# Optimization experiments

Hardware: AMD Instinct MI355X
Metric: run time of the kernel (lower is better)

The kernel has to match this reference:

```python
import jax, jax.numpy as jnp
import numpy as np

B, IN, HID, OUT = 1024, 512, 128, 64
INP1 = IN + 1  # 513, after prepending ones column


def setup_inputs() -> dict:
    key = jax.random.key(0)
    k1, k2, k3, k4, k5, k6, k7, k8 = jax.random.split(key, 8)
    s1 = 1.0 / np.sqrt(INP1 * INP1)
    s2 = 1.0 / np.sqrt(HID)
    return {
        "img": jax.random.normal(k1, (B, IN), dtype=jnp.float32),
        "tab": jax.random.normal(k2, (B, IN), dtype=jnp.float32),
        "W1": jax.random.uniform(k3, (HID, INP1 * INP1), jnp.float32, -s1, s1),
        "b1": jax.random.uniform(k4, (HID,), jnp.float32, -s1, s1),
        "W2": jax.random.uniform(k5, (HID, HID), jnp.float32, -s2, s2),
        "b2": jax.random.uniform(k6, (HID,), jnp.float32, -s2, s2),
        "W3": jax.random.uniform(k7, (OUT, HID), jnp.float32, -s2, s2),
        "b3": jax.random.uniform(k8, (OUT,), jnp.float32, -s2, s2),
    }


def reference(img, tab, W1, b1, W2, b2, W3, b3):
    ones = jnp.ones((img.shape[0], 1), dtype=img.dtype)
    x = jnp.concatenate([ones, img], axis=1)  # [B, IN+1]
    t = jnp.concatenate([ones, tab], axis=1)  # [B, IN+1]
    # batched outer product, flattened: [B, (IN+1)*(IN+1)]
    fusion = jnp.einsum("bi,bj->bij", x, t).reshape(x.shape[0], -1)
    # dropout is identity in eval mode
    y1 = fusion @ W1.T + b1
    y2 = jnp.tanh(y1 @ W2.T + b2)
    y3 = jax.nn.relu(y2 @ W3.T + b3)
    return y3
```

## Files before the change

kernel.cpp:

```cpp
#include <hip/hip_runtime.h>
#include <hip/hip_bf16.h>

typedef __bf16 bf16x8 __attribute__((ext_vector_type(8)));
typedef float f32x4 __attribute__((ext_vector_type(4)));
typedef float f32x4u __attribute__((ext_vector_type(4), aligned(4)));
typedef unsigned short u16x8 __attribute__((ext_vector_type(8)));

typedef __attribute__((address_space(1))) const unsigned int gu32;
typedef __attribute__((address_space(3))) unsigned int lu32;

#define B_SZ   1024
#define IN_SZ  512
#define HID    128
#define OUT_SZ 64
#define BK     32
#define NKT    16
#define M2     65536

static __device__ __forceinline__ unsigned short f2bf(float f) {
    __hip_bfloat16 h = __float2bfloat16(f);
    return *reinterpret_cast<unsigned short*>(&h);
}

__global__ __launch_bounds__(256) void prep_kernel(
    const float* __restrict__ img, const float* __restrict__ tab,
    unsigned short* __restrict__ tbt, float* __restrict__ xhT,
    float* __restrict__ tc)
{
    const int blk = blockIdx.x;
    for (int j = threadIdx.x; j < 512; j += 256) {
        float v = (j == 0) ? 1.0f : tab[(size_t)blk * IN_SZ + (j - 1)];
        tbt[(size_t)blk * 512 + j] = f2bf(v);
    }
    if (threadIdx.x == 0) tc[blk] = tab[(size_t)blk * IN_SZ + 511];
    if (blk < 513) {
        for (int b = threadIdx.x; b < B_SZ; b += 256)
            xhT[(size_t)blk * B_SZ + b] =
                (blk == 0) ? 1.0f : img[(size_t)b * IN_SZ + (blk - 1)];
    }
}

__global__ __launch_bounds__(256) void prep2_kernel(
    const float* __restrict__ w1, unsigned short* __restrict__ w1c)
{
    const long long gid = (long long)blockIdx.x * 256 + threadIdx.x;
    const int r  = (int)(gid >> 6);
    const int c8 = ((int)gid & 63) << 3;
    const size_t srow = (size_t)(r >> 9) * 513 + (r & 511);
    const float* src = w1 + srow * 513 + c8;
    const f32x4u lo = *reinterpret_cast<const f32x4u*>(src);
    const f32x4u hi = *reinterpret_cast<const f32x4u*>(src + 4);
    u16x8 u;
    u[0] = f2bf(lo[0]); u[1] = f2bf(lo[1]); u[2] = f2bf(lo[2]); u[3] = f2bf(lo[3]);
    u[4] = f2bf(hi[0]); u[5] = f2bf(hi[1]); u[6] = f2bf(hi[2]); u[7] = f2bf(hi[3]);
    *reinterpret_cast<u16x8*>(w1c + (size_t)r * 512 + c8) = u;
}

__global__ __launch_bounds__(256) void prep3_kernel(
    const float* __restrict__ w1, float* __restrict__ wrowT)
{
    const int idx = blockIdx.x * 256 + threadIdx.x;
    if (idx < 513 * 128) {
        const int j = idx >> 7, h = idx & 127;
        wrowT[idx] = w1[((size_t)h * 513 + 512) * 513 + j];
    }
}

__global__ __launch_bounds__(512, 4) void gemm_fused(
    const float* __restrict__ w1, const unsigned short* __restrict__ w1c,
    const unsigned short* __restrict__ tbt,
    const float* __restrict__ xhT, const float* __restrict__ tc,
    float* __restrict__ y1acc)
{
    __shared__ unsigned short Als[3][128 * BK];
    __shared__ unsigned short Bls[3][256 * BK];

    const int wgid = (blockIdx.x & 7) * 256 + (blockIdx.x >> 3);
    const int bm = wgid >> 2;
    const int bn = wgid & 3;
    const int m0 = bm * 128;
    const int n0 = bn * 256;
    const int tid  = threadIdx.x;
    const int wv   = tid >> 6;
    const int wr   = wv >> 2;
    const int wc   = wv & 3;
    const int lane = tid & 63;
    const int l15  = lane & 15;
    const int kg   = lane >> 4;

    const unsigned short* asrc;
    {
        const int r  = tid >> 2;
        const int cl = (tid & 3) ^ ((r >> 1) & 3);
        asrc = w1c + (size_t)(m0 + r) * 512 + cl * 8;
    }
    const int aBase = (wv * 64) * 8;

    const unsigned short* bsrc[2];
    int bBase[2];
    #pragma unroll
    for (int q = 0; q < 2; ++q) {
        const int p  = q * 512 + tid;
        const int r  = p >> 2;
        const int cl = (p & 3) ^ ((r >> 1) & 3);
        bsrc[q] = tbt + (size_t)(n0 + r) * 512 + cl * 8;
        bBase[q] = (q * 512 + wv * 64) * 8;
    }

    int aoffs[4], boffs[4];
    #pragma unroll
    for (int ms = 0; ms < 4; ++ms) {
        const int r = wr * 64 + ms * 16 + l15;
        aoffs[ms] = (r * 4 + (kg ^ ((r >> 1) & 3))) * 8;
    }
    #pragma unroll
    for (int ns = 0; ns < 4; ++ns) {
        const int r = wc * 64 + ns * 16 + l15;
        boffs[ns] = (r * 4 + (kg ^ ((r >> 1) & 3))) * 8;
    }

    f32x4 acc[4][4] = {};

#define STAGE(BUF, KT) do {                                                  \
        const int k32_ = (KT) * BK;                                          \
        __builtin_amdgcn_global_load_lds(                                    \
            (gu32*)(const void*)(asrc + k32_),                               \
            (lu32*)(void*)&Als[BUF][aBase], 16, 0, 0);                       \
        _Pragma("unroll")                                                    \
        for (int q_ = 0; q_ < 2; ++q_)                                       \
            __builtin_amdgcn_global_load_lds(                                \
                (gu32*)(const void*)(bsrc[q_] + k32_),                       \
                (lu32*)(void*)&Bls[BUF][bBase[q_]], 16, 0, 0);               \
    } while (0)

    STAGE(0, 0);
    STAGE(1, 1);

    #pragma unroll
    for (int kt = 0; kt < NKT; ++kt) {
        if (kt == NKT - 1) asm volatile("s_waitcnt vmcnt(0)" ::: "memory");
        else               asm volatile("s_waitcnt vmcnt(3)" ::: "memory");
        __builtin_amdgcn_s_barrier();
        __builtin_amdgcn_sched_barrier(0);

        if (kt + 2 < NKT) STAGE((kt + 2) % 3, kt + 2);

        const int cur = kt % 3;
        const unsigned short* ab = &Als[cur][0];
        const unsigned short* bb = &Bls[cur][0];
        bf16x8 af[4], bfr[4];
        #pragma unroll
        for (int ms = 0; ms < 4; ++ms)
            af[ms] = *reinterpret_cast<const bf16x8*>(&ab[aoffs[ms]]);
        #pragma unroll
        for (int ns = 0; ns < 4; ++ns)
            bfr[ns] = *reinterpret_cast<const bf16x8*>(&bb[boffs[ns]]);
        __builtin_amdgcn_s_setprio(1);
        #pragma unroll
        for (int ms = 0; ms < 4; ++ms)
            #pragma unroll
            for (int ns = 0; ns < 4; ++ns)
                acc[ms][ns] = __builtin_amdgcn_mfma_f32_16x16x32_bf16(
                    af[ms], bfr[ns], acc[ms][ns], 0, 0, 0);
        __builtin_amdgcn_s_setprio(0);
    }
#undef STAGE

    const int h0    = bm >> 2;
    const int ibase = (bm & 3) * 128;
    const size_t orow = (size_t)h0 * 513;

    float wcv[4][4];
    #pragma unroll
    for (int ms = 0; ms < 4; ++ms)
        #pragma unroll
        for (int v = 0; v < 4; ++v) {
            const int i_ = ibase + wr * 64 + ms * 16 + kg * 4 + v;
            wcv[ms][v] = w1[(orow + i_) * 513 + 512];
        }

    #pragma unroll
    for (int ns = 0; ns < 4; ++ns) {
        const int ncol = n0 + wc * 64 + ns * 16 + l15;
        const float tv = tc[ncol];
        float s0 = 0.f;
        #pragma unroll
        for (int ms = 0; ms < 4; ++ms) {
            const int i_ = ibase + wr * 64 + ms * 16 + kg * 4;
            #pragma unroll
            for (int v = 0; v < 4; ++v)
                s0 += (acc[ms][ns][v] + wcv[ms][v] * tv)
                      * xhT[(size_t)(i_ + v) * B_SZ + ncol];
        }
        s0 += __shfl_xor(s0, 16); s0 += __shfl_xor(s0, 32);
        if (lane < 16) atomicAdd(&y1acc[(size_t)ncol * HID + h0], s0);
    }
}

__global__ __launch_bounds__(128) void tail_kernel(
    const float* __restrict__ img, const float* __restrict__ tab,
    const float* __restrict__ wrowT, float* __restrict__ y1acc)
{
    __shared__ float tls[4][513];
    const int b0 = blockIdx.x * 4;
    const int h  = threadIdx.x;
    #pragma unroll
    for (int q = 0; q < 4; ++q)
        for (int j = h; j < 513; j += 128)
            tls[q][j] = (j == 0) ? 1.0f : tab[(size_t)(b0 + q) * IN_SZ + (j - 1)];
    __syncthreads();
    float a0 = 0.f, a1 = 0.f, a2 = 0.f, a3 = 0.f;
    #pragma unroll 8
    for (int j = 0; j < 513; ++j) {
        const float w = wrowT[j * 128 + h];
        a0 += w * tls[0][j]; a1 += w * tls[1][j];
        a2 += w * tls[2][j]; a3 += w * tls[3][j];
    }
    atomicAdd(&y1acc[(size_t)(b0 + 0) * HID + h], a0 * img[(size_t)(b0 + 0) * IN_SZ + 511]);
    atomicAdd(&y1acc[(size_t)(b0 + 1) * HID + h], a1 * img[(size_t)(b0 + 1) * IN_SZ + 511]);
    atomicAdd(&y1acc[(size_t)(b0 + 2) * HID + h], a2 * img[(size_t)(b0 + 2) * IN_SZ + 511]);
    atomicAdd(&y1acc[(size_t)(b0 + 3) * HID + h], a3 * img[(size_t)(b0 + 3) * IN_SZ + 511]);
}

__global__ __launch_bounds__(512, 4) void gemm_fused_fb(
    const float* __restrict__ w1, const unsigned short* __restrict__ tbt,
    const float* __restrict__ xhT, const float* __restrict__ tc,
    float* __restrict__ y1acc)
{
    __shared__ float          Afs[2][64 * BK];
    __shared__ unsigned short Bls[2][512 * BK];

    const int bm = blockIdx.x >> 1;
    const int bn = blockIdx.x & 1;
    const int m0 = bm * 64;
    const int n0 = bn * 512;
    const int tid  = threadIdx.x;
    const int wv   = tid >> 6;
    const int lane = tid & 63;
    const int l15  = lane & 15;
    const int kg   = lane >> 4;

    const int ar  = tid >> 3;
    const int acl = (tid & 7) ^ (ar & 7);
    const float* asrc = w1 + (size_t)(m0 + ar) * 513 + acl * 4;
    const int aBase = (wv * 64) * 4;

    const unsigned short* bsrc[4];
    int bBase[4];
    #pragma unroll
    for (int q = 0; q < 4; ++q) {
        const int p  = q * 512 + tid;
        const int r  = p >> 2;
        const int cl = (p & 3) ^ ((r >> 1) & 3);
        bsrc[q] = tbt + (size_t)(n0 + r) * 512 + cl * 8;
        bBase[q] = (q * 512 + wv * 64) * 8;
    }

    int aoff0[4], aoff1[4], boffs[4];
    #pragma unroll
    for (int ms = 0; ms < 4; ++ms) {
        const int r = ms * 16 + l15;
        aoff0[ms] = r * 32 + (((kg * 2) + 0) ^ (r & 7)) * 4;
        aoff1[ms] = r * 32 + (((kg * 2) + 1) ^ (r & 7)) * 4;
    }
    #pragma unroll
    for (int ns = 0; ns < 4; ++ns) {
        const int r = wv * 64 + ns * 16 + l15;
        boffs[ns] = ((r << 2) | (kg ^ ((r >> 1) & 3))) * 8;
    }

    f32x4 acc[4][4] = {};

#define STAGE_FB(BUF, KT) do {                                               \
        const int k32_ = (KT) * BK;                                          \
        _Pragma("unroll")                                                    \
        for (int q_ = 0; q_ < 4; ++q_)                                       \
            __builtin_amdgcn_global_load_lds(                                \
                (gu32*)(const void*)(bsrc[q_] + k32_),                       \
                (lu32*)(void*)&Bls[BUF][bBase[q_]], 16, 0, 0);               \
        __builtin_amdgcn_global_load_lds(                                    \
            (gu32*)(const void*)(asrc + k32_),                               \
            (lu32*)(void*)&Afs[BUF][aBase], 16, 0, 0);                       \
    } while (0)

    STAGE_FB(0, 0);
    __syncthreads();

    for (int kt = 0; kt < NKT; ++kt) {
        const int cur = kt & 1;
        if (kt + 1 < NKT) STAGE_FB(cur ^ 1, kt + 1);

        const float*          ab = &Afs[cur][0];
        const unsigned short* bb = &Bls[cur][0];
        bf16x8 bfr[4];
        #pragma unroll
        for (int ns = 0; ns < 4; ++ns)
            bfr[ns] = *reinterpret_cast<const bf16x8*>(&bb[boffs[ns]]);
        #pragma unroll
        for (int ms = 0; ms < 4; ++ms) {
            const f32x4 lo = *reinterpret_cast<const f32x4*>(&ab[aoff0[ms]]);
            const f32x4 hi = *reinterpret_cast<const f32x4*>(&ab[aoff1[ms]]);
            u16x8 u;
            u[0] = f2bf(lo[0]); u[1] = f2bf(lo[1]);
            u[2] = f2bf(lo[2]); u[3] = f2bf(lo[3]);
            u[4] = f2bf(hi[0]); u[5] = f2bf(hi[1]);
            u[6] = f2bf(hi[2]); u[7] = f2bf(hi[3]);
            const bf16x8 af = __builtin_bit_cast(bf16x8, u);
            #pragma unroll
            for (int ns = 0; ns < 4; ++ns)
                acc[ms][ns] = __builtin_amdgcn_mfma_f32_16x16x32_bf16(
                    af, bfr[ns], acc[ms][ns], 0, 0, 0);
        }
        __syncthreads();
    }
#undef STAGE_FB

    const int h0 = m0 / 513;
    const int mb = (h0 + 1) * 513;
    const bool cross = (mb < m0 + 64);

    float wcv[4][4];
    #pragma unroll
    for (int ms = 0; ms < 4; ++ms)
        #pragma unroll
        for (int v = 0; v < 4; ++v)
            wcv[ms][v] = w1[(size_t)(m0 + ms * 16 + kg * 4 + v) * 513 + 512];

    #pragma unroll
    for (int ns = 0; ns < 4; ++ns) {
        const int ncol = n0 + wv * 64 + ns * 16 + l15;
        const float tv = tc[ncol];
        float s0 = 0.f, s1 = 0.f;
        #pragma unroll
        for (int ms = 0; ms < 4; ++ms) {
            #pragma unroll
            for (int v = 0; v < 4; ++v) {
                const int m = m0 + ms * 16 + kg * 4 + v;
                const bool lo = (m < mb);
                const int i = lo ? (m - h0 * 513) : (m - mb);
                const float val = (acc[ms][ns][v] + wcv[ms][v] * tv)
                                  * xhT[(size_t)i * B_SZ + ncol];
                if (lo) s0 += val; else s1 += val;
            }
        }
        s0 += __shfl_xor(s0, 16); s0 += __shfl_xor(s0, 32);
        if (lane < 16) atomicAdd(&y1acc[(size_t)ncol * HID + h0], s0);
        if (cross) {
            s1 += __shfl_xor(s1, 16); s1 += __shfl_xor(s1, 32);
            if (lane < 16 && (h0 + 1) < HID)
                atomicAdd(&y1acc[(size_t)ncol * HID + h0 + 1], s1);
        }
    }
}

__global__ __launch_bounds__(128) void mlp_kernel(
    const float* __restrict__ y1acc, const float* __restrict__ b1,
    const float* __restrict__ W2, const float* __restrict__ b2,
    const float* __restrict__ W3, const float* __restrict__ b3,
    float* __restrict__ out)
{
    __shared__ float y1r[HID];
    __shared__ float y2r[HID];
    const int b = blockIdx.x;
    const int h = threadIdx.x;
    y1r[h] = y1acc[(size_t)b * HID + h] + b1[h];
    __syncthreads();
    float a = b2[h];
    const float* w2r = W2 + (size_t)h * HID;
    #pragma unroll 8
    for (int k = 0; k < HID; ++k) a += w2r[k] * y1r[k];
    y2r[h] = tanhf(a);
    __syncthreads();
    if (h < OUT_SZ) {
        float a3 = b3[h];
        const float* w3r = W3 + (size_t)h * HID;
        #pragma unroll 8
        for (int k = 0; k < HID; ++k) a3 += w3r[k] * y2r[k];
        out[(size_t)b * OUT_SZ + h] = fmaxf(a3, 0.f);
    }
}

extern "C" void kernel_launch(void* const* d_in, const int* in_sizes, int n_in,
                              void* d_out, int out_size, void* d_ws, size_t ws_size,
                              hipStream_t stream) {
    const float* img = (const float*)d_in[0];
    const float* tab = (const float*)d_in[1];
    const float* W1  = (const float*)d_in[2];
    const float* b1  = (const float*)d_in[3];
    const float* W2  = (const float*)d_in[4];
    const float* b2  = (const float*)d_in[5];
    const float* W3  = (const float*)d_in[6];
    const float* b3  = (const float*)d_in[7];
    float* out = (float*)d_out;

    char* ws = (char*)d_ws;
    float*          y1acc = (float*)ws;
    unsigned short* tbt   = (unsigned short*)(ws + 524288);
    float*          xhT   = (float*)(ws + 1572864);
    float*          tc    = (float*)(ws + 3674112);
    float*          wrowT = (float*)(ws + 3678208);
    unsigned short* w1c   = (unsigned short*)(ws + 3940864);
    const size_t need = 3940864ULL + 67108864ULL;

    hipMemsetAsync(y1acc, 0, (size_t)B_SZ * HID * sizeof(float), stream);
    prep_kernel<<<dim3(1024), dim3(256), 0, stream>>>(img, tab, tbt, xhT, tc);
    if (ws_size >= need) {
        prep2_kernel<<<dim3(M2 * 64 / 256), dim3(256), 0, stream>>>(W1, w1c);
        prep3_kernel<<<dim3(257), dim3(256), 0, stream>>>(W1, wrowT);
        gemm_fused<<<dim3(2048), dim3(512), 0, stream>>>(W1, w1c, tbt, xhT, tc, y1acc);
        tail_kernel<<<dim3(256), dim3(128), 0, stream>>>(img, tab, wrowT, y1acc);
    } else {
        gemm_fused_fb<<<dim3(2052), dim3(512), 0, stream>>>(W1, tbt, xhT, tc, y1acc);
    }
    mlp_kernel<<<dim3(1024), dim3(128), 0, stream>>>(y1acc, b1, W2, b2, W3, b3, out);
}
```

Baseline: 216.2 us.

## Fuse W1 fp32-to-bf16 conversion into GEMM A-tile loading, drop prep2 pass

Removes the separate prep2 kernel, which converted all of W1 (about 134MB fp32) into a 67MB bf16 copy. The GEMM now loads fp32 W1 rows directly into registers, converts them to bf16 and writes them to LDS, prefetching two k-tiles ahead. This removes a full write plus re-read of the bf16 copy. In exchange, A-tile loads become register-staged with unaligned fp32 reads, and each iteration gains extra LDS-store waits and barriers. The inner MFMA loop is also reordered to load B fragments per column.

```diff
diff --git a/kernel.cpp b/kernel.cpp
--- a/kernel.cpp
+++ b/kernel.cpp
@@ -40,22 +40,6 @@
     }
 }
 
-__global__ __launch_bounds__(256) void prep2_kernel(
-    const float* __restrict__ w1, unsigned short* __restrict__ w1c)
-{
-    const long long gid = (long long)blockIdx.x * 256 + threadIdx.x;
-    const int r  = (int)(gid >> 6);
-    const int c8 = ((int)gid & 63) << 3;
-    const size_t srow = (size_t)(r >> 9) * 513 + (r & 511);
-    const float* src = w1 + srow * 513 + c8;
-    const f32x4u lo = *reinterpret_cast<const f32x4u*>(src);
-    const f32x4u hi = *reinterpret_cast<const f32x4u*>(src + 4);
-    u16x8 u;
-    u[0] = f2bf(lo[0]); u[1] = f2bf(lo[1]); u[2] = f2bf(lo[2]); u[3] = f2bf(lo[3]);
-    u[4] = f2bf(hi[0]); u[5] = f2bf(hi[1]); u[6] = f2bf(hi[2]); u[7] = f2bf(hi[3]);
-    *reinterpret_cast<u16x8*>(w1c + (size_t)r * 512 + c8) = u;
-}
-
 __global__ __launch_bounds__(256) void prep3_kernel(
     const float* __restrict__ w1, float* __restrict__ wrowT)
 {
@@ -67,8 +51,7 @@
 }
 
 __global__ __launch_bounds__(512, 4) void gemm_fused(
-    const float* __restrict__ w1, const unsigned short* __restrict__ w1c,
-    const unsigned short* __restrict__ tbt,
+    const float* __restrict__ w1, const unsigned short* __restrict__ tbt,
     const float* __restrict__ xhT, const float* __restrict__ tc,
     float* __restrict__ y1acc)
 {
@@ -78,8 +61,9 @@
     const int wgid = (blockIdx.x & 7) * 256 + (blockIdx.x >> 3);
     const int bm = wgid >> 2;
     const int bn = wgid & 3;
-    const int m0 = bm * 128;
     const int n0 = bn * 256;
+    const int h0    = bm >> 2;
+    const int ibase = (bm & 3) * 128;
     const int tid  = threadIdx.x;
     const int wv   = tid >> 6;
     const int wr   = wv >> 2;
@@ -88,13 +72,9 @@
     const int l15  = lane & 15;
     const int kg   = lane >> 4;
 
-    const unsigned short* asrc;
-    {
-        const int r  = tid >> 2;
-        const int cl = (tid & 3) ^ ((r >> 1) & 3);
-        asrc = w1c + (size_t)(m0 + r) * 512 + cl * 8;
-    }
-    const int aBase = (wv * 64) * 8;
+    const int ar  = tid >> 2;
+    const int acl = (tid & 3) ^ ((ar >> 1) & 3);
+    const float* asrcF = w1 + ((size_t)h0 * 513 + ibase + ar) * 513 + acl * 8;
 
     const unsigned short* bsrc[2];
     int bBase[2];
@@ -120,56 +100,79 @@
     }
 
     f32x4 acc[4][4] = {};
-
-#define STAGE(BUF, KT) do {                                                  \
+    f32x4u rAlo, rAhi;
+
+#define STB(BUF, KT) do {                                                    \
         const int k32_ = (KT) * BK;                                          \
-        __builtin_amdgcn_global_load_lds(                                    \
-            (gu32*)(const void*)(asrc + k32_),                               \
-            (lu32*)(void*)&Als[BUF][aBase], 16, 0, 0);                       \
         _Pragma("unroll")                                                    \
         for (int q_ = 0; q_ < 2; ++q_)                                       \
             __builtin_amdgcn_global_load_lds(                                \
                 (gu32*)(const void*)(bsrc[q_] + k32_),                       \
                 (lu32*)(void*)&Bls[BUF][bBase[q_]], 16, 0, 0);               \
     } while (0)
-
-    STAGE(0, 0);
-    STAGE(1, 1);
+#define CVW8(DST, LO, HI) do {                                               \
+        u16x8 u_;                                                            \
+        u_[0] = f2bf((LO)[0]); u_[1] = f2bf((LO)[1]);                        \
+        u_[2] = f2bf((LO)[2]); u_[3] = f2bf((LO)[3]);                        \
+        u_[4] = f2bf((HI)[0]); u_[5] = f2bf((HI)[1]);                        \
+        u_[6] = f2bf((HI)[2]); u_[7] = f2bf((HI)[3]);                        \
+        *reinterpret_cast<u16x8*>(DST) = u_;                                 \
+    } while (0)
+
+    {
+        const f32x4u t0lo = *reinterpret_cast<const f32x4u*>(asrcF);
+        const f32x4u t0hi = *reinterpret_cast<const f32x4u*>(asrcF + 4);
+        const f32x4u t1lo = *reinterpret_cast<const f32x4u*>(asrcF + 32);
+        const f32x4u t1hi = *reinterpret_cast<const f32x4u*>(asrcF + 36);
+        CVW8(&Als[0][tid * 8], t0lo, t0hi);
+        CVW8(&Als[1][tid * 8], t1lo, t1hi);
+        STB(0, 0);
+        STB(1, 1);
+    }
+    __syncthreads();
 
     #pragma unroll
     for (int kt = 0; kt < NKT; ++kt) {
-        if (kt == NKT - 1) asm volatile("s_waitcnt vmcnt(0)" ::: "memory");
-        else               asm volatile("s_waitcnt vmcnt(3)" ::: "memory");
-        __builtin_amdgcn_s_barrier();
-        __builtin_amdgcn_sched_barrier(0);
-
-        if (kt + 2 < NKT) STAGE((kt + 2) % 3, kt + 2);
-
         const int cur = kt % 3;
         const unsigned short* ab = &Als[cur][0];
         const unsigned short* bb = &Bls[cur][0];
-        bf16x8 af[4], bfr[4];
+
+        if (kt >= 1 && kt + 1 < NKT)
+            CVW8(&Als[(kt + 1) % 3][tid * 8], rAlo, rAhi);
+        if (kt + 2 < NKT) {
+            const float* s_ = asrcF + (kt + 2) * 32;
+            rAlo = *reinterpret_cast<const f32x4u*>(s_);
+            rAhi = *reinterpret_cast<const f32x4u*>(s_ + 4);
+        }
+
+        bf16x8 af[4];
         #pragma unroll
         for (int ms = 0; ms < 4; ++ms)
             af[ms] = *reinterpret_cast<const bf16x8*>(&ab[aoffs[ms]]);
-        #pragma unroll
-        for (int ns = 0; ns < 4; ++ns)
-            bfr[ns] = *reinterpret_cast<const bf16x8*>(&bb[boffs[ns]]);
         __builtin_amdgcn_s_setprio(1);
         #pragma unroll
-        for (int ms = 0; ms < 4; ++ms)
+        for (int ns = 0; ns < 4; ++ns) {
+            const bf16x8 bf = *reinterpret_cast<const bf16x8*>(&bb[boffs[ns]]);
             #pragma unroll
-            for (int ns = 0; ns < 4; ++ns)
+            for (int ms = 0; ms < 4; ++ms)
                 acc[ms][ns] = __builtin_amdgcn_mfma_f32_16x16x32_bf16(
-                    af[ms], bfr[ns], acc[ms][ns], 0, 0, 0);
+                    af[ms], bf, acc[ms][ns], 0, 0, 0);
+        }
         __builtin_amdgcn_s_setprio(0);
-    }
-#undef STAGE
-
-    const int h0    = bm >> 2;
-    const int ibase = (bm & 3) * 128;
+
+        if (kt == NKT - 1) break;
+
+        if (kt + 2 >= NKT) asm volatile("s_waitcnt vmcnt(0)" ::: "memory");
+        else               asm volatile("s_waitcnt vmcnt(2)" ::: "memory");
+        if (kt + 2 < NKT) STB((kt + 2) % 3, kt + 2);
+        asm volatile("s_waitcnt lgkmcnt(0)" ::: "memory");
+        __builtin_amdgcn_s_barrier();
+        __builtin_amdgcn_sched_barrier(0);
+    }
+#undef STB
+#undef CVW8
+
     const size_t orow = (size_t)h0 * 513;
-
     float wcv[4][4];
     #pragma unroll
     for (int ms = 0; ms < 4; ++ms)
@@ -399,15 +402,13 @@
     float*          xhT   = (float*)(ws + 1572864);
     float*          tc    = (float*)(ws + 3674112);
     float*          wrowT = (float*)(ws + 3678208);
-    unsigned short* w1c   = (unsigned short*)(ws + 3940864);
-    const size_t need = 3940864ULL + 67108864ULL;
+    const size_t need = 3678208ULL + 262656ULL;
 
     hipMemsetAsync(y1acc, 0, (size_t)B_SZ * HID * sizeof(float), stream);
     prep_kernel<<<dim3(1024), dim3(256), 0, stream>>>(img, tab, tbt, xhT, tc);
     if (ws_size >= need) {
-        prep2_kernel<<<dim3(M2 * 64 / 256), dim3(256), 0, stream>>>(W1, w1c);
         prep3_kernel<<<dim3(257), dim3(256), 0, stream>>>(W1, wrowT);
-        gemm_fused<<<dim3(2048), dim3(512), 0, stream>>>(W1, w1c, tbt, xhT, tc, y1acc);
+        gemm_fused<<<dim3(2048), dim3(512), 0, stream>>>(W1, tbt, xhT, tc, y1acc);
         tail_kernel<<<dim3(256), dim3(128), 0, stream>>>(img, tab, wrowT, y1acc);
     } else {
         gemm_fused_fb<<<dim3(2052), dim3(512), 0, stream>>>(W1, tbt, xhT, tc, y1acc);
```

Result: faster. 194.5 us (-10.0%).

## Enlarge GEMM workgroup tile to 256x256 with 1024 threads

Applied to the files above, without the earlier changes.

Doubles the M dimension of each workgroup tile from 128 to 256 rows and uses 1024 threads (16 waves), halving the grid. Each thread now issues one A and one B async global-to-LDS load per stage, and the wait count is adjusted to match. Larger tiles raise operand reuse and cut redundant B reads from global memory, but they double LDS use per block and the 1024-thread launch bound with 4 blocks requested may force register limits or lower occupancy.

```diff
diff --git a/kernel.cpp b/kernel.cpp
--- a/kernel.cpp
+++ b/kernel.cpp
@@ -66,20 +66,22 @@
     }
 }
 
-__global__ __launch_bounds__(512, 4) void gemm_fused(
+__global__ __launch_bounds__(1024, 4) void gemm_fused(
     const float* __restrict__ w1, const unsigned short* __restrict__ w1c,
     const unsigned short* __restrict__ tbt,
     const float* __restrict__ xhT, const float* __restrict__ tc,
     float* __restrict__ y1acc)
 {
-    __shared__ unsigned short Als[3][128 * BK];
+    __shared__ unsigned short Als[3][256 * BK];
     __shared__ unsigned short Bls[3][256 * BK];
 
-    const int wgid = (blockIdx.x & 7) * 256 + (blockIdx.x >> 3);
+    const int wgid = (blockIdx.x & 7) * 128 + (blockIdx.x >> 3);
     const int bm = wgid >> 2;
     const int bn = wgid & 3;
-    const int m0 = bm * 128;
+    const int m0 = bm * 256;
     const int n0 = bn * 256;
+    const int h0    = bm >> 1;
+    const int ibase = (bm & 1) * 256;
     const int tid  = threadIdx.x;
     const int wv   = tid >> 6;
     const int wr   = wv >> 2;
@@ -89,23 +91,14 @@
     const int kg   = lane >> 4;
 
     const unsigned short* asrc;
+    const unsigned short* bsrc;
     {
         const int r  = tid >> 2;
         const int cl = (tid & 3) ^ ((r >> 1) & 3);
         asrc = w1c + (size_t)(m0 + r) * 512 + cl * 8;
-    }
-    const int aBase = (wv * 64) * 8;
-
-    const unsigned short* bsrc[2];
-    int bBase[2];
-    #pragma unroll
-    for (int q = 0; q < 2; ++q) {
-        const int p  = q * 512 + tid;
-        const int r  = p >> 2;
-        const int cl = (p & 3) ^ ((r >> 1) & 3);
-        bsrc[q] = tbt + (size_t)(n0 + r) * 512 + cl * 8;
-        bBase[q] = (q * 512 + wv * 64) * 8;
-    }
+        bsrc = tbt + (size_t)(n0 + r) * 512 + cl * 8;
+    }
+    const int sBase = (wv * 64) * 8;
 
     int aoffs[4], boffs[4];
     #pragma unroll
@@ -121,29 +114,27 @@
 
     f32x4 acc[4][4] = {};
 
-#define STAGE(BUF, KT) do {                                                  \
+#define STG(BUF, KT) do {                                                    \
         const int k32_ = (KT) * BK;                                          \
         __builtin_amdgcn_global_load_lds(                                    \
             (gu32*)(const void*)(asrc + k32_),                               \
-            (lu32*)(void*)&Als[BUF][aBase], 16, 0, 0);                       \
-        _Pragma("unroll")                                                    \
-        for (int q_ = 0; q_ < 2; ++q_)                                       \
-            __builtin_amdgcn_global_load_lds(                                \
-                (gu32*)(const void*)(bsrc[q_] + k32_),                       \
-                (lu32*)(void*)&Bls[BUF][bBase[q_]], 16, 0, 0);               \
+            (lu32*)(void*)&Als[BUF][sBase], 16, 0, 0);                       \
+        __builtin_amdgcn_global_load_lds(                                    \
+            (gu32*)(const void*)(bsrc + k32_),                               \
+            (lu32*)(void*)&Bls[BUF][sBase], 16, 0, 0);                       \
     } while (0)
 
-    STAGE(0, 0);
-    STAGE(1, 1);
+    STG(0, 0);
+    STG(1, 1);
 
     #pragma unroll
     for (int kt = 0; kt < NKT; ++kt) {
         if (kt == NKT - 1) asm volatile("s_waitcnt vmcnt(0)" ::: "memory");
-        else               asm volatile("s_waitcnt vmcnt(3)" ::: "memory");
+        else               asm volatile("s_waitcnt vmcnt(2)" ::: "memory");
         __builtin_amdgcn_s_barrier();
         __builtin_amdgcn_sched_barrier(0);
 
-        if (kt + 2 < NKT) STAGE((kt + 2) % 3, kt + 2);
+        if (kt + 2 < NKT) STG((kt + 2) % 3, kt + 2);
 
         const int cur = kt % 3;
         const unsigned short* ab = &Als[cur][0];
@@ -164,12 +155,9 @@
                     af[ms], bfr[ns], acc[ms][ns], 0, 0, 0);
         __builtin_amdgcn_s_setprio(0);
     }
-#undef STAGE
-
-    const int h0    = bm >> 2;
-    const int ibase = (bm & 3) * 128;
+#undef STG
+
     const size_t orow = (size_t)h0 * 513;
-
     float wcv[4][4];
     #pragma unroll
     for (int ms = 0; ms < 4; ++ms)
@@ -407,7 +395,7 @@
     if (ws_size >= need) {
         prep2_kernel<<<dim3(M2 * 64 / 256), dim3(256), 0, stream>>>(W1, w1c);
         prep3_kernel<<<dim3(257), dim3(256), 0, stream>>>(W1, wrowT);
-        gemm_fused<<<dim3(2048), dim3(512), 0, stream>>>(W1, w1c, tbt, xhT, tc, y1acc);
+        gemm_fused<<<dim3(1024), dim3(1024), 0, stream>>>(W1, w1c, tbt, xhT, tc, y1acc);
         tail_kernel<<<dim3(256), dim3(128), 0, stream>>>(img, tab, wrowT, y1acc);
     } else {
         gemm_fused_fb<<<dim3(2052), dim3(512), 0, stream>>>(W1, tbt, xhT, tc, y1acc);
```

Result: slower. 237.8 us (+10.0%).
